# Optimization experiments

Measured on AMD Instinct MI355X. Metric: run time of the kernel, lower is better.

The kernel has to match this reference:

```python
import jax, jax.numpy as jnp
import numpy as np
from jax import lax

# config (matches init_kwargs)
NUM_CLASSES = 10
SCORE_THRESH = 0.05
TOPK = 1000
DET_PER_IMG = 100
NMS_SCORE = 0.3
NMS_SIGMA = 0.5
IMG_H, IMG_W = 800.0, 1333.0
IOU_SUPPRESS = 0.8
BBOX_XFORM_CLIP = float(np.log(1000.0 / 16.0))
EPS = 1e-7


def setup_inputs() -> dict:
    key = jax.random.key(0)
    k1, k2, k3 = jax.random.split(key, 3)
    B, A, C = 8, 200000, NUM_CLASSES
    cls_logits = jax.random.normal(k1, (B, A, C), dtype=jnp.float32)
    bbox_regression = 0.5 * jax.random.normal(k2, (B, A, 4), dtype=jnp.float32)
    # plausible anchors: random centers + sizes inside the image, xyxy format
    u = jax.random.uniform(k3, (A, 6), dtype=jnp.float32)
    cx = u[:, 0] * IMG_W
    cy = u[:, 1] * IMG_H
    w = 16.0 + u[:, 2] * 200.0
    h = 16.0 + u[:, 3] * 200.0
    anchors = jnp.stack([cx - 0.5 * w, cy - 0.5 * h, cx + 0.5 * w, cy + 0.5 * h], axis=-1)
    return {"cls_logits": cls_logits, "bbox_regression": bbox_regression, "anchors": anchors}


def _decode(rel, anc):
    # torchvision BoxCoder.decode_single, weights (1,1,1,1). rel, anc: [K,4] xyxy anchors
    wa = anc[:, 2] - anc[:, 0]
    ha = anc[:, 3] - anc[:, 1]
    cxa = anc[:, 0] + 0.5 * wa
    cya = anc[:, 1] + 0.5 * ha
    dx, dy = rel[:, 0], rel[:, 1]
    dw = jnp.minimum(rel[:, 2], BBOX_XFORM_CLIP)
    dh = jnp.minimum(rel[:, 3], BBOX_XFORM_CLIP)
    cx = dx * wa + cxa
    cy = dy * ha + cya
    w = jnp.exp(dw) * wa
    h = jnp.exp(dh) * ha
    boxes = jnp.stack([cx - 0.5 * w, cy - 0.5 * h, cx + 0.5 * w, cy + 0.5 * h], axis=-1)
    # clip_boxes_to_image
    x = jnp.clip(boxes[:, 0::2], 0.0, IMG_W)
    y = jnp.clip(boxes[:, 1::2], 0.0, IMG_H)
    return jnp.stack([x[:, 0], y[:, 0], x[:, 1], y[:, 1]], axis=-1)


def _iou_one(box, boxes):
    # box [4] vs boxes [K,4] -> [K]
    lt = jnp.maximum(box[:2], boxes[:, :2])
    rb = jnp.minimum(box[2:], boxes[:, 2:])
    wh = jnp.clip(rb - lt, 0.0)
    inter = wh[:, 0] * wh[:, 1]
    a1 = (box[2] - box[0]) * (box[3] - box[1])
    a2 = (boxes[:, 2] - boxes[:, 0]) * (boxes[:, 3] - boxes[:, 1])
    return inter / (a1 + a2 - inter + EPS)


def _postprocess_one(logits, rel, anchors):
    # logits [A,C], rel [A,4], anchors [A,4]
    probs = jax.nn.sigmoid(logits)
    scores_all = jnp.max(probs, axis=-1)               # [A]
    labels_all = jnp.argmax(probs, axis=-1)            # [A]
    scores_all = jnp.where(scores_all > SCORE_THRESH, scores_all, 0.0)
    top_scores, top_idx = lax.top_k(scores_all, TOPK)  # [K]
    labels = labels_all[top_idx]
    boxes = _decode(rel[top_idx], anchors[top_idx])    # [K,4]

    K = TOPK
    # --- batched gaussian soft-NMS (same-label decay only) ---
    def soft_step(carry, _):
        sc, out = carry
        i = jnp.argmax(sc)
        s = sc[i]
        out = out.at[i].set(jnp.maximum(s, 0.0))
        ious = _iou_one(boxes[i], boxes)
        decay = jnp.where(labels == labels[i], jnp.exp(-(ious ** 2) / NMS_SIGMA), 1.0)
        sc = (sc * decay).at[i].set(-1.0)
        return (sc, out), None
    (_, decayed), _ = lax.scan(soft_step, (top_scores, jnp.zeros_like(top_scores)), None, length=K)
    keep = decayed > NMS_SCORE

    # --- sort by decayed score desc, greedy hard suppression at IoU>0.8 ---
    order = jnp.argsort(-decayed)
    b = boxes[order]
    s = decayed[order]
    l = labels[order]
    alive0 = keep[order]
    idxs = jnp.arange(K)

    def greedy_step(alive, i):
        ious = _iou_one(b[i], b)
        suppress = (ious > IOU_SUPPRESS) & (idxs > i)
        alive = jnp.where(alive[i], alive & ~suppress, alive)
        return alive, None
    alive, _ = lax.scan(greedy_step, alive0, idxs)

    final_scores = jnp.where(alive, s, -1.0)
    out_scores, out_i = lax.top_k(final_scores, DET_PER_IMG)  # preserves desc order of survivors
    return b[out_i], out_scores, l[out_i]


def reference(cls_logits, bbox_regression, anchors):
    boxes, scores, labels = jax.vmap(_postprocess_one, in_axes=(0, 0, None))(
        cls_logits, bbox_regression, anchors)
    return boxes, scores, labels  # [B,D,4], [B,D], [B,D] (score -1 = padding)
```

## Files before the change

### kernel.cpp

```cpp
#include <hip/hip_runtime.h>
#include <math.h>

#define NCLS 10
#define TOPK 1000
#define DETS 100
#define CANDMAX 4096
#define SLOTS 16
#define ACTK 256

#define BIN0 0x3D4Cu
#define NBINS 576
#define NBLK 64

__device__ __forceinline__ float sigmoidf_(float x) {
    return 1.0f / (1.0f + expf(-x));
}

__device__ __forceinline__ float key_score(const unsigned long long* key, int c) {
    return __uint_as_float(~(unsigned)(key[c] >> 32));
}

__device__ __forceinline__ unsigned fkey_(float f) {
    unsigned b = __float_as_uint(f);
    return (b & 0x80000000u) ? ~b : (b | 0x80000000u);
}
__device__ __forceinline__ float funkey_(unsigned k) {
    return __uint_as_float((k & 0x80000000u) ? (k & 0x7FFFFFFFu) : ~k);
}

__device__ __forceinline__ unsigned wave_umax_(unsigned x) {
    unsigned t;
    t = (unsigned)__builtin_amdgcn_update_dpp(0, (int)x, 0x111, 0xF, 0xF, false); x = (x > t) ? x : t;
    t = (unsigned)__builtin_amdgcn_update_dpp(0, (int)x, 0x112, 0xF, 0xF, false); x = (x > t) ? x : t;
    t = (unsigned)__builtin_amdgcn_update_dpp(0, (int)x, 0x114, 0xF, 0xF, false); x = (x > t) ? x : t;
    t = (unsigned)__builtin_amdgcn_update_dpp(0, (int)x, 0x118, 0xF, 0xF, false); x = (x > t) ? x : t;
    t = (unsigned)__builtin_amdgcn_update_dpp(0, (int)x, 0x142, 0xF, 0xF, false); x = (x > t) ? x : t;
    t = (unsigned)__builtin_amdgcn_update_dpp(0, (int)x, 0x143, 0xF, 0xF, false); x = (x > t) ? x : t;
    return (unsigned)__builtin_amdgcn_readlane((int)x, 63);
}

__global__ __launch_bounds__(256) void k_score_hist(const float* __restrict__ logits,
                                                    float* __restrict__ scores,
                                                    unsigned* hist,
                                                    unsigned* __restrict__ done,
                                                    unsigned* __restrict__ P,
                                                    int A, int use_scores) {
    __shared__ unsigned h[NBINS];
    __shared__ int s_last;
    int img = blockIdx.y;
    for (int i = threadIdx.x; i < NBINS; i += 256) h[i] = 0;
    __syncthreads();

    const float* base = logits + (size_t)img * A * NCLS;
    int nquad = A >> 2;
    for (int q = blockIdx.x * 256 + threadIdx.x; q < nquad; q += NBLK * 256) {
        const float4* lp = (const float4*)(base + (size_t)q * 40);
        float f[40];
#pragma unroll
        for (int i = 0; i < 10; ++i) ((float4*)f)[i] = lp[i];
        float4 s4;
        float* sv = &s4.x;
#pragma unroll
        for (int j = 0; j < 4; ++j) {
            float m = f[10 * j];
#pragma unroll
            for (int c = 1; c < 10; ++c) m = fmaxf(m, f[10 * j + c]);
            float sc = sigmoidf_(m);
            sc = (sc > 0.05f) ? sc : 0.0f;
            sv[j] = sc;
            if (sc > 0.0f) {
                unsigned bin = (__float_as_uint(sc) >> 16) - BIN0;
                if (bin >= NBINS) bin = NBINS - 1;
                atomicAdd(&h[bin], 1u);
            }
        }
        if (use_scores) ((float4*)(scores + (size_t)img * A))[q] = s4;
    }
    int tail0 = nquad << 2;
    if (blockIdx.x == 0) {
        for (int a = tail0 + (int)threadIdx.x; a < A; a += 256) {
            const float* lp2 = base + (size_t)a * NCLS;
            float m = lp2[0];
            for (int c = 1; c < 10; ++c) m = fmaxf(m, lp2[c]);
            float sc = sigmoidf_(m);
            sc = (sc > 0.05f) ? sc : 0.0f;
            if (use_scores) scores[(size_t)img * A + a] = sc;
            if (sc > 0.0f) {
                unsigned bin = (__float_as_uint(sc) >> 16) - BIN0;
                if (bin >= NBINS) bin = NBINS - 1;
                atomicAdd(&h[bin], 1u);
            }
        }
    }
    __syncthreads();
    for (int i = threadIdx.x; i < NBINS; i += 256) {
        unsigned c = h[i];
        if (c) atomicAdd(&hist[(size_t)img * NBINS + i], c);
    }
    __syncthreads();
    if (threadIdx.x == 0) {
        __threadfence();
        unsigned old = atomicAdd(&done[img], 1u);
        s_last = (old == (unsigned)(NBLK - 1)) ? 1 : 0;
    }
    __syncthreads();
    if (s_last && threadIdx.x < 64) {
        int lane = threadIdx.x;
        unsigned* hh = hist + (size_t)img * NBINS;
        unsigned b[9];
        unsigned s = 0;
#pragma unroll
        for (int j = 0; j < 9; ++j) { b[j] = atomicAdd(&hh[lane * 9 + j], 0u); s += b[j]; }
        unsigned suf = s;
#pragma unroll
        for (int d = 1; d < 64; d <<= 1) {
            unsigned o = __shfl_down(suf, d);
            if (lane + d < 64) suf += o;
        }
        unsigned above = __shfl_down(suf, 1);
        if (lane == 63) above = 0;
        if (lane == 0 && suf < (unsigned)TOPK) P[img] = 0u;
        if (above < (unsigned)TOPK && suf >= (unsigned)TOPK) {
            unsigned cum = above;
            for (int j = 8; j >= 0; --j) {
                cum += b[j];
                if (cum >= (unsigned)TOPK) { P[img] = BIN0 + (unsigned)(lane * 9 + j); break; }
            }
        }
    }
}

__global__ __launch_bounds__(256) void k_compact(const float* __restrict__ logits,
                                                 const float* __restrict__ scores,
                                                 const unsigned* __restrict__ P,
                                                 unsigned* __restrict__ ctr,
                                                 unsigned long long* __restrict__ cand,
                                                 int A) {
    int img = blockIdx.y;
    unsigned p = P[img];
    int lane = threadIdx.x & 63;
    int nquad = A >> 2;
    for (int q = blockIdx.x * 256 + threadIdx.x; q < nquad; q += NBLK * 256) {
        float sv[4];
        if (scores) {
            float4 t = ((const float4*)(scores + (size_t)img * A))[q];
            sv[0] = t.x; sv[1] = t.y; sv[2] = t.z; sv[3] = t.w;
        } else {
            const float* lp = logits + ((size_t)img * A + (size_t)q * 4) * NCLS;
            float f[40];
#pragma unroll
            for (int i = 0; i < 10; ++i) ((float4*)f)[i] = ((const float4*)lp)[i];
#pragma unroll
            for (int j = 0; j < 4; ++j) {
                float m = f[10 * j];
#pragma unroll
                for (int c = 1; c < 10; ++c) m = fmaxf(m, f[10 * j + c]);
                float sc = sigmoidf_(m);
                sv[j] = (sc > 0.05f) ? sc : 0.0f;
            }
        }
#pragma unroll
        for (int j = 0; j < 4; ++j) {
            unsigned bits = __float_as_uint(sv[j]);
            bool take = (bits >> 16) >= p;
            unsigned long long mask = __ballot(take);
            if (mask) {
                int cnt = __popcll(mask);
                int leader = __ffsll((unsigned long long)mask) - 1;
                unsigned pos = 0;
                if (lane == leader) pos = atomicAdd(&ctr[img], (unsigned)cnt);
                pos = (unsigned)__shfl((int)pos, leader);
                if (take) {
                    unsigned slot = pos + (unsigned)__popcll(mask & ((1ull << lane) - 1ull));
                    if (slot < CANDMAX) {
                        unsigned a = (unsigned)(q * 4 + j);
                        cand[(size_t)img * CANDMAX + slot] =
                            ((unsigned long long)bits << 32) | (unsigned)(~a);
                    }
                }
            }
        }
    }
    int tail0 = nquad << 2;
    if (blockIdx.x == 0) {
        for (int a = tail0 + (int)threadIdx.x; a < A; a += 256) {
            float sc;
            if (scores) sc = scores[(size_t)img * A + a];
            else {
                const float* lp = logits + ((size_t)img * A + a) * NCLS;
                float m = lp[0];
                for (int c = 1; c < 10; ++c) m = fmaxf(m, lp[c]);
                float s = sigmoidf_(m);
                sc = (s > 0.05f) ? s : 0.0f;
            }
            unsigned bits = __float_as_uint(sc);
            if ((bits >> 16) >= p) {
                unsigned pos = atomicAdd(&ctr[img], 1u);
                if (pos < CANDMAX)
                    cand[(size_t)img * CANDMAX + pos] =
                        ((unsigned long long)bits << 32) | (unsigned)(~a);
            }
        }
    }
}

__global__ __launch_bounds__(1024) void k_sortnms(const unsigned long long* __restrict__ cand,
                                                  const unsigned* __restrict__ ctr,
                                                  const float* __restrict__ logits,
                                                  const float* __restrict__ rel,
                                                  const float* __restrict__ anch,
                                                  float* __restrict__ out, int A, int B) {
    __shared__ unsigned long long key[CANDMAX];
    __shared__ float s_box[TOPK][4];
    __shared__ int   s_lab[TOPK];
    __shared__ float s_pbox[TOPK][4];
    __shared__ int   s_plab[TOPK];
    __shared__ float s_psc[TOPK];
    __shared__ int   s_alive[TOPK];

    const float CLIPV = 4.135166556742356f;
    const float EPS = 1e-7f;
    const float W_ = 1333.0f, H_ = 800.0f;

    int img = blockIdx.x;
    int tid = threadIdx.x;

    unsigned n = ctr[img];
    if (n > CANDMAX) n = CANDMAX;
    int L = (n <= 1024) ? 1024 : (n <= 2048) ? 2048 : CANDMAX;
    for (int i = tid; i < L; i += 1024)
        key[i] = (i < (int)n) ? ~cand[(size_t)img * CANDMAX + i] : ~0ull;
    __syncthreads();
    for (int k = 2; k <= L; k <<= 1) {
        for (int j = k >> 1; j > 0; j >>= 1) {
            for (int i = tid; i < L; i += 1024) {
                int l = i ^ j;
                if (l > i) {
                    unsigned long long va = key[i], vb = key[l];
                    bool up = ((i & k) == 0);
                    if (up ? (va > vb) : (va < vb)) { key[i] = vb; key[l] = va; }
                }
            }
            __syncthreads();
        }
    }
    for (int i = L + tid; i < CANDMAX; i += 1024) key[i] = ~0ull;
    __syncthreads();

    if (tid < TOPK) {
        unsigned long long ik = key[tid];
        unsigned ai = (unsigned)ik;
        if (ai >= (unsigned)A) ai = 0;
        const float* lp = logits + ((size_t)img * A + ai) * NCLS;
        float best = sigmoidf_(lp[0]); int lbb = 0;
#pragma unroll
        for (int cc = 1; cc < NCLS; ++cc) {
            float v = sigmoidf_(lp[cc]);
            if (v > best) { best = v; lbb = cc; }
        }
        const float* rp = rel + ((size_t)img * A + ai) * 4;
        const float* ap = anch + (size_t)ai * 4;
        float a0 = ap[0], a1 = ap[1], a2 = ap[2], a3 = ap[3];
        float wa = a2 - a0, ha = a3 - a1;
        float cxa = a0 + 0.5f * wa, cya = a1 + 0.5f * ha;
        float dx = rp[0], dy = rp[1];
        float dw = fminf(rp[2], CLIPV), dh = fminf(rp[3], CLIPV);
        float cx = dx * wa + cxa, cy = dy * ha + cya;
        float w = expf(dw) * wa, h = expf(dh) * ha;
        s_box[tid][0] = fminf(fmaxf(cx - 0.5f * w, 0.0f), W_);
        s_box[tid][1] = fminf(fmaxf(cy - 0.5f * h, 0.0f), H_);
        s_box[tid][2] = fminf(fmaxf(cx + 0.5f * w, 0.0f), W_);
        s_box[tid][3] = fminf(fmaxf(cy + 0.5f * h, 0.0f), H_);
        s_lab[tid] = lbb;
    }
    __syncthreads();
    if (tid >= 64) return;
    int lane = tid;

    int M = TOPK;
    int need_full = 0;
    float bound = key_score(key, ACTK);

    {
        float sc[4], x1[4], y1[4], x2[4], y2[4], ar[4];
        int lb[4];
#pragma unroll
        for (int j = 0; j < 4; ++j) {
            int c = lane + (j << 6);
            float4 bb = *(const float4*)&s_box[c][0];
            x1[j] = bb.x; y1[j] = bb.y; x2[j] = bb.z; y2[j] = bb.w;
            ar[j] = (bb.z - bb.x) * (bb.w - bb.y);
            lb[j] = s_lab[c];
            sc[j] = key_score(key, c);
        }

        int nconf = 0, Mf = -1;

        for (int t = 0; t < ACTK; ++t) {
            float bv = sc[0]; int bj = 0;
#pragma unroll
            for (int j = 1; j < 4; ++j)
                if (sc[j] > bv) { bv = sc[j]; bj = j; }
            unsigned mk = fkey_(bv);
            unsigned mx = wave_umax_(mk);
            float pcur = funkey_(mx);

            if (!(pcur >= bound)) { need_full = 1; break; }

            int pick = -1;
#pragma unroll
            for (int jj = 0; jj < 4; ++jj) {
                if (pick < 0) {
                    unsigned long long mj = __ballot(mk == mx && bj == jj);
                    if (mj) pick = (jj << 6) + (__ffsll(mj) - 1);
                }
            }

            float psc = fmaxf(pcur, 0.0f);
            float4 pb = *(const float4*)&s_box[pick][0];
            int plab_ = s_lab[pick];
            if (lane == 0) {
                *(float4*)&s_pbox[t][0] = pb;
                s_plab[t] = plab_;
                s_psc[t] = psc;
            }

            float4 qb[4]; int ga[4];
#pragma unroll
            for (int k = 0; k < 4; ++k) {
                int p = lane + (k << 6);
                int pc2 = (p < t) ? p : 0;
                qb[k] = *(const float4*)&s_pbox[pc2][0];
                ga[k] = (p < t) ? s_alive[pc2] : 0;
            }

            float wax = (pb.z - pb.x) * (pb.w - pb.y);
#pragma unroll
            for (int j = 0; j < 4; ++j) {
                float lx2 = fmaxf(pb.x, x1[j]), ly2 = fmaxf(pb.y, y1[j]);
                float rx2 = fminf(pb.z, x2[j]), ry2 = fminf(pb.w, y2[j]);
                float iw2 = fmaxf(rx2 - lx2, 0.0f), ih2 = fmaxf(ry2 - ly2, 0.0f);
                float inter2 = iw2 * ih2;
                bool hot = (inter2 > 0.0f) && (lb[j] == plab_);
                if (__ballot(hot) != 0ull) {
                    float iou2 = inter2 / (wax + ar[j] - inter2 + EPS);
                    float ie = (lb[j] == plab_) ? iou2 : 0.0f;
                    sc[j] *= expf(-(ie * ie) / 0.5f);
                }
            }
#pragma unroll
            for (int j = 0; j < 4; ++j)
                if (lane + (j << 6) == pick) sc[j] = -1.0f;

            bool sup = false;
#pragma unroll
            for (int k = 0; k < 4; ++k) {
                if (ga[k]) {
                    float lx = fmaxf(pb.x, qb[k].x), ly = fmaxf(pb.y, qb[k].y);
                    float rx = fminf(pb.z, qb[k].z), ry = fminf(pb.w, qb[k].w);
                    float iw = fmaxf(rx - lx, 0.0f), ih = fmaxf(ry - ly, 0.0f);
                    float inter = iw * ih;
                    float qa = (qb[k].z - qb[k].x) * (qb[k].w - qb[k].y);
                    float iou = inter / (wax + qa - inter + EPS);
                    sup = sup || (iou > 0.8f);
                }
            }
            bool alive = (psc > 0.3f) && (__ballot(sup) == 0ull);
            if (lane == 0) s_alive[t] = alive ? 1 : 0;
            nconf += alive ? 1 : 0;
            if (nconf >= DETS) { Mf = t + 1; break; }
        }
        if (!need_full) {
            if (Mf < 0) need_full = 1;
            else M = Mf;
        }
    }

    if (need_full) {
        float sc[SLOTS], x1[SLOTS], y1[SLOTS], x2[SLOTS], y2[SLOTS], ar[SLOTS];
        int lb[SLOTS];
#pragma unroll
        for (int j = 0; j < SLOTS; ++j) {
            int c = lane + (j << 6);
            if (c < TOPK) {
                float4 bb = *(const float4*)&s_box[c][0];
                x1[j] = bb.x; y1[j] = bb.y; x2[j] = bb.z; y2[j] = bb.w;
                ar[j] = (bb.z - bb.x) * (bb.w - bb.y);
                lb[j] = s_lab[c];
                sc[j] = key_score(key, c);
            } else {
                sc[j] = -2.0f; lb[j] = -1;
                x1[j] = y1[j] = x2[j] = y2[j] = ar[j] = 0.0f;
            }
        }
        unsigned long long aw = 0;
        if (lane < 15) aw = ~0ull;
        else if (lane == 15) aw = (1ull << (TOPK - 15 * 64)) - 1;
        int f = 0, nconf = 0;
        M = TOPK;
        for (int t = 0; t < TOPK; ++t) {
            int fp = (f < TOPK) ? f : 0;
            float4 fb = *(const float4*)&s_box[fp][0];
            int flab = s_lab[fp];
            int fs = f >> 6;
            float v = sc[0];
#pragma unroll
            for (int j = 1; j < SLOTS; ++j) if (fs == j) v = sc[j];
            float cf = __shfl(v, f & 63);
            float lm = sc[0];
#pragma unroll
            for (int j = 1; j < SLOTS; ++j) lm = fmaxf(lm, sc[j]);
            int pick; float pcur; float4 pb; int plab_;
            unsigned long long bb2 = __ballot(lm > cf);
            if (bb2 == 0) {
                pick = f; pcur = cf; pb = fb; plab_ = flab;
            } else {
                float bv = sc[0]; int bi = lane;
#pragma unroll
                for (int j = 1; j < SLOTS; ++j) {
                    int e = lane + (j << 6);
                    if (sc[j] > bv) { bv = sc[j]; bi = e; }
                }
#pragma unroll
                for (int d = 32; d; d >>= 1) {
                    float ov = __shfl_xor(bv, d);
                    int oi = __shfl_xor(bi, d);
                    if (ov > bv || (ov == bv && oi < bi)) { bv = ov; bi = oi; }
                }
                pick = bi; pcur = bv;
                pb = *(const float4*)&s_box[pick][0];
                plab_ = s_lab[pick];
            }
            float psc = fmaxf(pcur, 0.0f);
            if (lane == 0) {
                *(float4*)&s_pbox[t][0] = pb;
                s_plab[t] = plab_;
                s_psc[t] = psc;
            }
            bool alive = (psc > 0.3f);
            if (alive && t > 0) {
                float pa = (pb.z - pb.x) * (pb.w - pb.y);
                int kprev = ((t - 1) >> 6) + 1;
                bool sup = false;
                for (int k = 0; k < kprev; ++k) {
                    int p = lane + (k << 6);
                    int pc = (p < t) ? p : 0;
                    float4 qb = *(const float4*)&s_pbox[pc][0];
                    int ga = s_alive[pc];
                    if (p < t && ga) {
                        float lx = fmaxf(pb.x, qb.x), ly = fmaxf(pb.y, qb.y);
                        float rx = fminf(pb.z, qb.z), ry = fminf(pb.w, qb.w);
                        float iw = fmaxf(rx - lx, 0.0f), ih = fmaxf(ry - ly, 0.0f);
                        float inter = iw * ih;
                        float qa = (qb.z - qb.x) * (qb.w - qb.y);
                        float iou = inter / (pa + qa - inter + EPS);
                        sup = sup || (iou > 0.8f);
                    }
                }
                alive = (__ballot(sup) == 0ull);
            }
            if (lane == 0) s_alive[t] = alive ? 1 : 0;
            nconf += alive ? 1 : 0;
            if (nconf >= DETS) { M = t + 1; break; }
            float wax = (pb.z - pb.x) * (pb.w - pb.y);
#pragma unroll
            for (int j = 0; j < SLOTS; ++j) {
                float lx2 = fmaxf(pb.x, x1[j]), ly2 = fmaxf(pb.y, y1[j]);
                float rx2 = fminf(pb.z, x2[j]), ry2 = fminf(pb.w, y2[j]);
                float iw2 = fmaxf(rx2 - lx2, 0.0f), ih2 = fmaxf(ry2 - ly2, 0.0f);
                float inter2 = iw2 * ih2;
                bool hot = (inter2 > 0.0f) && (lb[j] == plab_);
                if (__ballot(hot) != 0ull) {
                    float iou2 = inter2 / (wax + ar[j] - inter2 + EPS);
                    float ie = (lb[j] == plab_) ? iou2 : 0.0f;
                    sc[j] *= expf(-(ie * ie) / 0.5f);
                }
            }
#pragma unroll
            for (int j = 0; j < SLOTS; ++j)
                if (lane + (j << 6) == pick) sc[j] = -1.0f;
            if (lane == (pick >> 6)) aw &= ~(1ull << (pick & 63));
            if (pick == f) {
                int fw = f >> 6;
                unsigned long long w2 = __shfl(aw, fw);
                while (w2 == 0ull && fw < 15) { ++fw; w2 = __shfl(aw, fw); }
                f = (w2 == 0ull) ? TOPK : (fw << 6) + (__ffsll(w2) - 1);
            }
        }
    }

    float* out_boxes  = out;
    float* out_scores = out + (size_t)B * DETS * 4;
    float* out_labels = out + (size_t)B * DETS * 5;
    int kmax = (M + 63) >> 6;
    int base = 0;
    for (int k = 0; k < kmax; ++k) {
        int p = lane + (k << 6);
        bool av = (p < M) && (s_alive[p] != 0);
        unsigned long long mask = __ballot(av);
        int slot = base + (int)__popcll(mask & ((1ull << lane) - 1ull));
        if (av && slot < DETS) {
            float4 pb = *(const float4*)&s_pbox[p][0];
            float* ob = out_boxes + ((size_t)img * DETS + slot) * 4;
            ob[0] = pb.x; ob[1] = pb.y; ob[2] = pb.z; ob[3] = pb.w;
            out_scores[img * DETS + slot] = s_psc[p];
            out_labels[img * DETS + slot] = (float)s_plab[p];
        }
        base += (int)__popcll(mask);
    }
    if (base < DETS) {
        int dbase = 0;
        for (int k = 0; k < kmax; ++k) {
            int p = lane + (k << 6);
            bool dd = (p < M) && (s_alive[p] == 0);
            unsigned long long mask = __ballot(dd);
            int slot = base + dbase + (int)__popcll(mask & ((1ull << lane) - 1ull));
            if (dd && slot < DETS) {
                float4 pb = *(const float4*)&s_pbox[p][0];
                float* ob = out_boxes + ((size_t)img * DETS + slot) * 4;
                ob[0] = pb.x; ob[1] = pb.y; ob[2] = pb.z; ob[3] = pb.w;
                out_scores[img * DETS + slot] = -1.0f;
                out_labels[img * DETS + slot] = (float)s_plab[p];
            }
            dbase += (int)__popcll(mask);
        }
    }
}

extern "C" void kernel_launch(void* const* d_in, const int* in_sizes, int n_in,
                              void* d_out, int out_size, void* d_ws, size_t ws_size,
                              hipStream_t stream) {
    const float* logits = (const float*)d_in[0];
    const float* rel = (const float*)d_in[1];
    const float* anch = (const float*)d_in[2];
    float* out = (float*)d_out;

    int A = in_sizes[2] / 4;
    int B = in_sizes[0] / (A * NCLS);

    char* w = (char*)d_ws;
    unsigned* hist = (unsigned*)w;           w += (size_t)B * NBINS * 4;
    unsigned* ctr = (unsigned*)w;            w += (size_t)B * 4;
    unsigned* done = (unsigned*)w;           w += (size_t)B * 4;
    size_t zbytes = (size_t)(w - (char*)d_ws);
    unsigned long long* cand = (unsigned long long*)w; w += (size_t)B * CANDMAX * 8;
    unsigned* P = (unsigned*)w;              w += (size_t)B * 4;
    w += 4;
    float* scores = (float*)w;
    size_t used = (size_t)(w - (char*)d_ws);
    int use_scores = (used + (size_t)B * A * 4 <= ws_size) ? 1 : 0;

    hipMemsetAsync(d_ws, 0, zbytes, stream);

    dim3 g1(NBLK, (unsigned)B);
    k_score_hist<<<g1, 256, 0, stream>>>(logits, scores, hist, done, P, A, use_scores);
    k_compact<<<g1, 256, 0, stream>>>(logits, use_scores ? scores : nullptr, P, ctr, cand, A);
    k_sortnms<<<B, 1024, 0, stream>>>(cand, ctr, logits, rel, anch, out, A, B);
}
```

Baseline: 275.5 us.

## Bin raw max logits into byte codes and recompute scores only for candidates

The score pass now maps the max logit straight to an 8-bit bin with a piecewise-linear rule, so the per-anchor sigmoid is gone. It writes one byte per anchor instead of a float score, and the shared histogram is spread over four replicas to cut atomic contention. The compaction pass reads only these bytes and reloads logits to recompute the exact sigmoid only for anchors it selects. In the NMS kernel the picked box is taken from registers with readlane instead of a shared-memory load. Risk: the coarser bins may admit more candidates and overflow CANDMAX, and the workspace no longer checks its size.

```diff
diff --git a/kernel.cpp b/kernel.cpp
--- a/kernel.cpp
+++ b/kernel.cpp
@@ -8,12 +8,23 @@
 #define SLOTS 16
 #define ACTK 256
 
-#define BIN0 0x3D4Cu
-#define NBINS 576
+#define NB2 256
+#define MGATE (-2.9444389791664403f)
+#define SEAM 2.2f
+#define SCA 30.907200f
+#define SCB 41.0f
 #define NBLK 64
 
 __device__ __forceinline__ float sigmoidf_(float x) {
     return 1.0f / (1.0f + expf(-x));
+}
+
+__device__ __forceinline__ int mbin_(float m) {
+    if (!(m > MGATE)) return 0;
+    int b;
+    if (m > SEAM) { b = 161 + (int)((m - SEAM) * SCB); if (b > 255) b = 255; }
+    else          { b = 1 + (int)((m - MGATE) * SCA);  if (b > 160) b = 160; }
+    return b;
 }
 
 __device__ __forceinline__ float key_score(const unsigned long long* key, int c) {
@@ -39,42 +50,38 @@
     return (unsigned)__builtin_amdgcn_readlane((int)x, 63);
 }
 
-__global__ __launch_bounds__(256) void k_score_hist(const float* __restrict__ logits,
-                                                    float* __restrict__ scores,
+__global__ __launch_bounds__(256) void k_score_bins(const float* __restrict__ logits,
+                                                    unsigned char* __restrict__ binc,
                                                     unsigned* hist,
                                                     unsigned* __restrict__ done,
                                                     unsigned* __restrict__ P,
-                                                    int A, int use_scores) {
-    __shared__ unsigned h[NBINS];
+                                                    int A) {
+    __shared__ unsigned h[4][NB2];
     __shared__ int s_last;
     int img = blockIdx.y;
-    for (int i = threadIdx.x; i < NBINS; i += 256) h[i] = 0;
+    for (int i = threadIdx.x; i < 4 * NB2; i += 256) ((unsigned*)h)[i] = 0;
     __syncthreads();
 
     const float* base = logits + (size_t)img * A * NCLS;
+    unsigned char* bc = binc + (size_t)img * A;
+    int rep = threadIdx.x & 3;
     int nquad = A >> 2;
     for (int q = blockIdx.x * 256 + threadIdx.x; q < nquad; q += NBLK * 256) {
         const float4* lp = (const float4*)(base + (size_t)q * 40);
         float f[40];
 #pragma unroll
         for (int i = 0; i < 10; ++i) ((float4*)f)[i] = lp[i];
-        float4 s4;
-        float* sv = &s4.x;
+        unsigned ub = 0;
 #pragma unroll
         for (int j = 0; j < 4; ++j) {
             float m = f[10 * j];
 #pragma unroll
             for (int c = 1; c < 10; ++c) m = fmaxf(m, f[10 * j + c]);
-            float sc = sigmoidf_(m);
-            sc = (sc > 0.05f) ? sc : 0.0f;
-            sv[j] = sc;
-            if (sc > 0.0f) {
-                unsigned bin = (__float_as_uint(sc) >> 16) - BIN0;
-                if (bin >= NBINS) bin = NBINS - 1;
-                atomicAdd(&h[bin], 1u);
-            }
-        }
-        if (use_scores) ((float4*)(scores + (size_t)img * A))[q] = s4;
+            int b = mbin_(m);
+            ub |= ((unsigned)b) << (8 * j);
+            if (b) atomicAdd(&h[rep][b], 1u);
+        }
+        *(unsigned*)(bc + (size_t)q * 4) = ub;
     }
     int tail0 = nquad << 2;
     if (blockIdx.x == 0) {
@@ -82,20 +89,15 @@
             const float* lp2 = base + (size_t)a * NCLS;
             float m = lp2[0];
             for (int c = 1; c < 10; ++c) m = fmaxf(m, lp2[c]);
-            float sc = sigmoidf_(m);
-            sc = (sc > 0.05f) ? sc : 0.0f;
-            if (use_scores) scores[(size_t)img * A + a] = sc;
-            if (sc > 0.0f) {
-                unsigned bin = (__float_as_uint(sc) >> 16) - BIN0;
-                if (bin >= NBINS) bin = NBINS - 1;
-                atomicAdd(&h[bin], 1u);
-            }
-        }
-    }
-    __syncthreads();
-    for (int i = threadIdx.x; i < NBINS; i += 256) {
-        unsigned c = h[i];
-        if (c) atomicAdd(&hist[(size_t)img * NBINS + i], c);
+            int b = mbin_(m);
+            bc[a] = (unsigned char)b;
+            if (b) atomicAdd(&h[rep][b], 1u);
+        }
+    }
+    __syncthreads();
+    for (int i = threadIdx.x; i < NB2; i += 256) {
+        unsigned c = h[0][i] + h[1][i] + h[2][i] + h[3][i];
+        if (c) atomicAdd(&hist[(size_t)img * NB2 + i], c);
     }
     __syncthreads();
     if (threadIdx.x == 0) {
@@ -106,11 +108,11 @@
     __syncthreads();
     if (s_last && threadIdx.x < 64) {
         int lane = threadIdx.x;
-        unsigned* hh = hist + (size_t)img * NBINS;
-        unsigned b[9];
+        unsigned* hh = hist + (size_t)img * NB2;
+        unsigned b4[4];
         unsigned s = 0;
 #pragma unroll
-        for (int j = 0; j < 9; ++j) { b[j] = atomicAdd(&hh[lane * 9 + j], 0u); s += b[j]; }
+        for (int j = 0; j < 4; ++j) { b4[j] = atomicAdd(&hh[lane * 4 + j], 0u); s += b4[j]; }
         unsigned suf = s;
 #pragma unroll
         for (int d = 1; d < 64; d <<= 1) {
@@ -122,47 +124,33 @@
         if (lane == 0 && suf < (unsigned)TOPK) P[img] = 0u;
         if (above < (unsigned)TOPK && suf >= (unsigned)TOPK) {
             unsigned cum = above;
-            for (int j = 8; j >= 0; --j) {
-                cum += b[j];
-                if (cum >= (unsigned)TOPK) { P[img] = BIN0 + (unsigned)(lane * 9 + j); break; }
+            for (int j = 3; j >= 0; --j) {
+                cum += b4[j];
+                if (cum >= (unsigned)TOPK) { P[img] = (unsigned)(lane * 4 + j); break; }
             }
         }
     }
 }
 
 __global__ __launch_bounds__(256) void k_compact(const float* __restrict__ logits,
-                                                 const float* __restrict__ scores,
+                                                 const unsigned char* __restrict__ binc,
                                                  const unsigned* __restrict__ P,
                                                  unsigned* __restrict__ ctr,
                                                  unsigned long long* __restrict__ cand,
                                                  int A) {
     int img = blockIdx.y;
     unsigned p = P[img];
+    unsigned psel = p ? (p - 1u) : 0u;
     int lane = threadIdx.x & 63;
+    const float* base = logits + (size_t)img * A * NCLS;
+    const unsigned* b4 = (const unsigned*)(binc + (size_t)img * A);
     int nquad = A >> 2;
     for (int q = blockIdx.x * 256 + threadIdx.x; q < nquad; q += NBLK * 256) {
-        float sv[4];
-        if (scores) {
-            float4 t = ((const float4*)(scores + (size_t)img * A))[q];
-            sv[0] = t.x; sv[1] = t.y; sv[2] = t.z; sv[3] = t.w;
-        } else {
-            const float* lp = logits + ((size_t)img * A + (size_t)q * 4) * NCLS;
-            float f[40];
-#pragma unroll
-            for (int i = 0; i < 10; ++i) ((float4*)f)[i] = ((const float4*)lp)[i];
-#pragma unroll
-            for (int j = 0; j < 4; ++j) {
-                float m = f[10 * j];
-#pragma unroll
-                for (int c = 1; c < 10; ++c) m = fmaxf(m, f[10 * j + c]);
-                float sc = sigmoidf_(m);
-                sv[j] = (sc > 0.05f) ? sc : 0.0f;
-            }
-        }
+        unsigned ub = b4[q];
 #pragma unroll
         for (int j = 0; j < 4; ++j) {
-            unsigned bits = __float_as_uint(sv[j]);
-            bool take = (bits >> 16) >= p;
+            unsigned bj = (ub >> (8 * j)) & 0xFFu;
+            bool take = (psel == 0u) || (bj >= psel);
             unsigned long long mask = __ballot(take);
             if (mask) {
                 int cnt = __popcll(mask);
@@ -174,6 +162,13 @@
                     unsigned slot = pos + (unsigned)__popcll(mask & ((1ull << lane) - 1ull));
                     if (slot < CANDMAX) {
                         unsigned a = (unsigned)(q * 4 + j);
+                        const float* lp = base + (size_t)a * NCLS;
+                        float m = lp[0];
+#pragma unroll
+                        for (int c = 1; c < 10; ++c) m = fmaxf(m, lp[c]);
+                        float sc = sigmoidf_(m);
+                        sc = (sc > 0.05f) ? sc : 0.0f;
+                        unsigned bits = __float_as_uint(sc);
                         cand[(size_t)img * CANDMAX + slot] =
                             ((unsigned long long)bits << 32) | (unsigned)(~a);
                     }
@@ -184,17 +179,14 @@
     int tail0 = nquad << 2;
     if (blockIdx.x == 0) {
         for (int a = tail0 + (int)threadIdx.x; a < A; a += 256) {
-            float sc;
-            if (scores) sc = scores[(size_t)img * A + a];
-            else {
-                const float* lp = logits + ((size_t)img * A + a) * NCLS;
+            unsigned bj = binc[(size_t)img * A + a];
+            if ((psel == 0u) || (bj >= psel)) {
+                const float* lp = base + (size_t)a * NCLS;
                 float m = lp[0];
                 for (int c = 1; c < 10; ++c) m = fmaxf(m, lp[c]);
-                float s = sigmoidf_(m);
-                sc = (s > 0.05f) ? s : 0.0f;
-            }
-            unsigned bits = __float_as_uint(sc);
-            if ((bits >> 16) >= p) {
+                float sc = sigmoidf_(m);
+                sc = (sc > 0.05f) ? sc : 0.0f;
+                unsigned bits = __float_as_uint(sc);
                 unsigned pos = atomicAdd(&ctr[img], 1u);
                 if (pos < CANDMAX)
                     cand[(size_t)img * CANDMAX + pos] =
@@ -316,9 +308,19 @@
                 }
             }
 
+            int jw = pick >> 6, wl = pick & 63;
+            float xs = x1[0], ys = y1[0], zs = x2[0], ws = y2[0]; int ls = lb[0];
+            if (jw == 1) { xs = x1[1]; ys = y1[1]; zs = x2[1]; ws = y2[1]; ls = lb[1]; }
+            if (jw == 2) { xs = x1[2]; ys = y1[2]; zs = x2[2]; ws = y2[2]; ls = lb[2]; }
+            if (jw == 3) { xs = x1[3]; ys = y1[3]; zs = x2[3]; ws = y2[3]; ls = lb[3]; }
+            float4 pb;
+            pb.x = __int_as_float(__builtin_amdgcn_readlane(__float_as_int(xs), wl));
+            pb.y = __int_as_float(__builtin_amdgcn_readlane(__float_as_int(ys), wl));
+            pb.z = __int_as_float(__builtin_amdgcn_readlane(__float_as_int(zs), wl));
+            pb.w = __int_as_float(__builtin_amdgcn_readlane(__float_as_int(ws), wl));
+            int plab_ = __builtin_amdgcn_readlane(ls, wl);
+
             float psc = fmaxf(pcur, 0.0f);
-            float4 pb = *(const float4*)&s_box[pick][0];
-            int plab_ = s_lab[pick];
             if (lane == 0) {
                 *(float4*)&s_pbox[t][0] = pb;
                 s_plab[t] = plab_;
@@ -539,21 +541,18 @@
     int B = in_sizes[0] / (A * NCLS);
 
     char* w = (char*)d_ws;
-    unsigned* hist = (unsigned*)w;           w += (size_t)B * NBINS * 4;
+    unsigned* hist = (unsigned*)w;           w += (size_t)B * NB2 * 4;
     unsigned* ctr = (unsigned*)w;            w += (size_t)B * 4;
     unsigned* done = (unsigned*)w;           w += (size_t)B * 4;
     size_t zbytes = (size_t)(w - (char*)d_ws);
     unsigned long long* cand = (unsigned long long*)w; w += (size_t)B * CANDMAX * 8;
     unsigned* P = (unsigned*)w;              w += (size_t)B * 4;
-    w += 4;
-    float* scores = (float*)w;
-    size_t used = (size_t)(w - (char*)d_ws);
-    int use_scores = (used + (size_t)B * A * 4 <= ws_size) ? 1 : 0;
+    unsigned char* binc = (unsigned char*)w;
 
     hipMemsetAsync(d_ws, 0, zbytes, stream);
 
     dim3 g1(NBLK, (unsigned)B);
-    k_score_hist<<<g1, 256, 0, stream>>>(logits, scores, hist, done, P, A, use_scores);
-    k_compact<<<g1, 256, 0, stream>>>(logits, use_scores ? scores : nullptr, P, ctr, cand, A);
+    k_score_bins<<<g1, 256, 0, stream>>>(logits, binc, hist, done, P, A);
+    k_compact<<<g1, 256, 0, stream>>>(logits, binc, P, ctr, cand, A);
     k_sortnms<<<B, 1024, 0, stream>>>(cand, ctr, logits, rel, anch, out, A, B);
 }
```

Measured after the change: 273.0 us. About the same (-0.9%).
